# Kernel tuning notes

Measured on AMD Instinct MI355X. Metric: run time of the kernel, lower is better.

Reference implementation:

```python
import jax, jax.numpy as jnp
import numpy as np

N_NODES = 100000
N_EDGES = 1600000
IN_DIM = 128
HEADS = 2
OUT_DIM = 64


def setup_inputs() -> dict:
    key = jax.random.key(0)
    k1, k2, k3, k4, k5 = jax.random.split(key, 5)
    x = jax.random.normal(k1, (N_NODES, IN_DIM), dtype=jnp.float32)
    edge_index = jax.random.randint(k2, (2, N_EDGES), 0, N_NODES, dtype=jnp.int32)
    # xavier-uniform-ish scales
    W = jax.random.uniform(k3, (IN_DIM, HEADS * OUT_DIM), dtype=jnp.float32,
                           minval=-1.0, maxval=1.0) * (6.0 / (IN_DIM + HEADS * OUT_DIM)) ** 0.5
    attn_l = jax.random.uniform(k4, (HEADS, OUT_DIM), dtype=jnp.float32,
                                minval=-1.0, maxval=1.0) * (6.0 / (HEADS + OUT_DIM)) ** 0.5
    attn_r = jax.random.uniform(k5, (HEADS, OUT_DIM), dtype=jnp.float32,
                                minval=-1.0, maxval=1.0) * (6.0 / (HEADS + OUT_DIM)) ** 0.5
    return {"x": x, "edge_index": edge_index, "W": W, "attn_l": attn_l, "attn_r": attn_r}


def reference(x, edge_index, W, attn_l, attn_r):
    N = x.shape[0]
    h = (x @ W).reshape(N, HEADS, OUT_DIM)          # [N,H,D]
    src, dst = edge_index[0], edge_index[1]          # [E]
    h_src = h[src]                                   # [E,H,D] gather
    h_dst = h[dst]                                   # [E,H,D] gather
    # per-edge, per-head attention logits
    alpha = jnp.einsum('ehd,hd->eh', h_src, attn_l) + jnp.einsum('ehd,hd->eh', h_dst, attn_r)
    alpha = jax.nn.leaky_relu(alpha, negative_slope=0.2)
    # NOTE: faithful to original torch code: softmax over dim=0 (ALL edges per head)
    alpha = jax.nn.softmax(alpha, axis=0)            # [E,H]
    msg = h_src * alpha[:, :, None]                  # [E,H,D]
    out = jnp.zeros((N, HEADS, OUT_DIM), dtype=h.dtype).at[dst].add(msg)
    return out.reshape(N, HEADS * OUT_DIM)
```

## Files before the change

### kernel.cpp

```cpp
#include <hip/hip_runtime.h>
#include <hip/hip_fp16.h>
#include <math.h>

#define IN_DIM   128
#define HEADS    2
#define OUT_DIM  64
#define OCOLS    128
#define BSHIFT   7
#define NPB      128
#define MAXB     1024
#define CAPF     2560
#define PARTB    512
#define CHUNK_MAX 3200
#define LOG2E    1.4426950408889634f

typedef __attribute__((ext_vector_type(4))) _Float16 half4v;
typedef __attribute__((ext_vector_type(8))) _Float16 half8v;
typedef __attribute__((ext_vector_type(4))) float    floatx4;

__global__ __launch_bounds__(256) void pack_w_kernel(
    const float* __restrict__ W, half8v* __restrict__ wpack) {
  int t = threadIdx.x;
  for (int s = t; s < 2048; s += 256) {
    int l = s & 63, ct = (s >> 6) & 7, kk = s >> 9;
    int q = l >> 4, n = l & 15;
    int c = ct * 16 + n;
    half8v f;
#pragma unroll
    for (int j = 0; j < 8; j++) {
      f[j] = (_Float16)W[(size_t)(kk * 32 + q * 8 + j) * OCOLS + c];
    }
    wpack[s] = f;
  }
}

__global__ __launch_bounds__(256) void gemm_kernel(
    const float* __restrict__ x, const half8v* __restrict__ wpack,
    const float* __restrict__ attn_l, const float* __restrict__ attn_r,
    _Float16* __restrict__ h16, float* __restrict__ alr, int N) {
  __shared__ half8v Wlds[2048];
  __shared__ __align__(16) _Float16 hstage[64 * OCOLS];
  const int tid = threadIdx.x;
  for (int i = tid; i < 2048; i += 256) Wlds[i] = wpack[i];

  const int wave = tid >> 6, lane = tid & 63;
  const int q = lane >> 4, m = lane & 15;
  const int rbase = blockIdx.x * 64 + wave * 16;
  const int arow = rbase + m;
  const bool rok = arow < N;

  half8v a[4];
#pragma unroll
  for (int kk = 0; kk < 4; kk++) {
    float4 u = rok ? *(const float4*)&x[(size_t)arow * IN_DIM + kk * 32 + q * 8]
                   : make_float4(0.f, 0.f, 0.f, 0.f);
    float4 v = rok ? *(const float4*)&x[(size_t)arow * IN_DIM + kk * 32 + q * 8 + 4]
                   : make_float4(0.f, 0.f, 0.f, 0.f);
    a[kk][0] = (_Float16)u.x; a[kk][1] = (_Float16)u.y;
    a[kk][2] = (_Float16)u.z; a[kk][3] = (_Float16)u.w;
    a[kk][4] = (_Float16)v.x; a[kk][5] = (_Float16)v.y;
    a[kk][6] = (_Float16)v.z; a[kk][7] = (_Float16)v.w;
  }
  __syncthreads();

  floatx4 acc[8];
#pragma unroll
  for (int ct = 0; ct < 8; ct++) {
    floatx4 c = {0.f, 0.f, 0.f, 0.f};
#pragma unroll
    for (int kk = 0; kk < 4; kk++) {
      c = __builtin_amdgcn_mfma_f32_16x16x32_f16(
          a[kk], Wlds[(kk * 8 + ct) * 64 + lane], c, 0, 0, 0);
    }
    acc[ct] = c;
  }

  float Al[8], Ar[8];
#pragma unroll
  for (int ct = 0; ct < 8; ct++) {
    Al[ct] = attn_l[ct * 16 + m];
    Ar[ct] = attn_r[ct * 16 + m];
  }
#pragma unroll
  for (int r = 0; r < 4; r++) {
    float al0 = 0.f, al1 = 0.f, ar0 = 0.f, ar1 = 0.f;
#pragma unroll
    for (int ct = 0; ct < 4; ct++) {
      al0 += acc[ct][r] * Al[ct];
      ar0 += acc[ct][r] * Ar[ct];
      al1 += acc[ct + 4][r] * Al[ct + 4];
      ar1 += acc[ct + 4][r] * Ar[ct + 4];
    }
#pragma unroll
    for (int off = 1; off < 16; off <<= 1) {
      al0 += __shfl_xor(al0, off);
      al1 += __shfl_xor(al1, off);
      ar0 += __shfl_xor(ar0, off);
      ar1 += __shfl_xor(ar1, off);
    }
    int orow = rbase + q * 4 + r;
    if (m == 0 && orow < N) {
      *(float4*)&alr[(size_t)orow * 4] =
          make_float4(al0 * LOG2E, al1 * LOG2E, ar0 * LOG2E, ar1 * LOG2E);
    }
  }

#pragma unroll
  for (int ct = 0; ct < 8; ct++) {
#pragma unroll
    for (int r = 0; r < 4; r++) {
      hstage[(wave * 16 + q * 4 + r) * OCOLS + ct * 16 + m] = (_Float16)acc[ct][r];
    }
  }
  __syncthreads();
  {
    int srow = tid >> 2, seg = tid & 3;
    int grow = blockIdx.x * 64 + srow;
    if (grow < N) {
      const int4* s = (const int4*)&hstage[srow * OCOLS + seg * 32];
      int4* d = (int4*)&h16[(size_t)grow * OCOLS + seg * 32];
      int4 v0 = s[0], v1 = s[1], v2 = s[2], v3 = s[3];
      d[0] = v0; d[1] = v1; d[2] = v2; d[3] = v3;
    }
  }
}

__device__ inline void softmax_comb(float& m, float& s, float m2, float s2) {
  float M = fmaxf(m, m2);
  s = s * __builtin_amdgcn_exp2f(m - M) + s2 * __builtin_amdgcn_exp2f(m2 - M);
  m = M;
}

__global__ __launch_bounds__(512) void alpha_part_kernel(
    const int* __restrict__ src, const int* __restrict__ dst,
    const float* __restrict__ alr, float* __restrict__ partials,
    int* __restrict__ gcur, unsigned int* __restrict__ pairs,
    int E, int nb1, int chunk) {
  __shared__ unsigned int pv[CHUNK_MAX];
  __shared__ unsigned short bk[CHUNK_MAX];
  __shared__ int hist[MAXB];
  __shared__ int cur[MAXB];
  const int t = threadIdx.x;
  const int base = blockIdx.x * chunk;
  const int lim = min(base + chunk, E);
  const int cntLoc = lim - base;

  for (int i = t; i < nb1; i += 512) hist[i] = 0;
  __syncthreads();

  const char* ab = (const char*)alr;
  float m0 = -1e30f, s0 = 0.f, m1 = -1e30f, s1 = 0.f;
  for (int e = base + t; e < lim; e += 512) {
    int sn = src[e], dn = dst[e];
    int li = e - base;
    pv[li] = (unsigned int)sn | ((unsigned int)(dn & (NPB - 1)) << 17);
    bk[li] = (unsigned short)(dn >> BSHIFT);
    atomicAdd(&hist[dn >> BSHIFT], 1);
    float4 as = *(const float4*)(ab + ((unsigned)sn << 4));
    float4 ad = *(const float4*)(ab + ((unsigned)dn << 4));
    float a0 = as.x + ad.z;
    float a1 = as.y + ad.w;
    a0 = (a0 > 0.f) ? a0 : 0.2f * a0;
    a1 = (a1 > 0.f) ? a1 : 0.2f * a1;
    {
      float M = fmaxf(m0, a0);
      s0 = s0 * __builtin_amdgcn_exp2f(m0 - M) + __builtin_amdgcn_exp2f(a0 - M);
      m0 = M;
    }
    {
      float M = fmaxf(m1, a1);
      s1 = s1 * __builtin_amdgcn_exp2f(m1 - M) + __builtin_amdgcn_exp2f(a1 - M);
      m1 = M;
    }
  }
  __syncthreads();
  for (int b = t; b < nb1; b += 512) {
    int h = hist[b];
    if (h) cur[b] = b * CAPF + atomicAdd(&gcur[b], h);
  }
  __syncthreads();
  for (int li = t; li < cntLoc; li += 512) {
    unsigned int p = pv[li];
    int bb = bk[li];
    int slot = atomicAdd(&cur[bb], 1);
    int cap = (bb + 1) * CAPF - 1;
    if (slot > cap) slot = cap;
    pairs[slot] = p;
  }
#pragma unroll
  for (int off = 1; off < 64; off <<= 1) {
    float m0o = __shfl_xor(m0, off), s0o = __shfl_xor(s0, off);
    float m1o = __shfl_xor(m1, off), s1o = __shfl_xor(s1, off);
    softmax_comb(m0, s0, m0o, s0o);
    softmax_comb(m1, s1, m1o, s1o);
  }
  __shared__ float red[8][4];
  int wave = t >> 6, lane = t & 63;
  if (lane == 0) {
    red[wave][0] = m0; red[wave][1] = s0; red[wave][2] = m1; red[wave][3] = s1;
  }
  __syncthreads();
  if (t == 0) {
    float M0 = red[0][0], S0 = red[0][1], M1 = red[0][2], S1 = red[0][3];
    for (int w = 1; w < 8; w++) {
      softmax_comb(M0, S0, red[w][0], red[w][1]);
      softmax_comb(M1, S1, red[w][2], red[w][3]);
    }
    float* p = &partials[(size_t)blockIdx.x * 4];
    p[0] = M0; p[1] = S0; p[2] = M1; p[3] = S1;
  }
}

__global__ __launch_bounds__(512) void stats_kernel(
    const float* __restrict__ partials, float* __restrict__ stats) {
  __shared__ float red[8][4];
  int t = threadIdx.x;
  float m0 = -1e30f, s0 = 0.f, m1 = -1e30f, s1 = 0.f;
  for (int i = t; i < PARTB; i += 512) {
    const float* p = &partials[(size_t)i * 4];
    softmax_comb(m0, s0, p[0], p[1]);
    softmax_comb(m1, s1, p[2], p[3]);
  }
#pragma unroll
  for (int off = 1; off < 64; off <<= 1) {
    float m0o = __shfl_xor(m0, off), s0o = __shfl_xor(s0, off);
    float m1o = __shfl_xor(m1, off), s1o = __shfl_xor(s1, off);
    softmax_comb(m0, s0, m0o, s0o);
    softmax_comb(m1, s1, m1o, s1o);
  }
  int wave = t >> 6, lane = t & 63;
  if (lane == 0) {
    red[wave][0] = m0; red[wave][1] = s0; red[wave][2] = m1; red[wave][3] = s1;
  }
  __syncthreads();
  if (t == 0) {
    float M0 = red[0][0], S0 = red[0][1], M1 = red[0][2], S1 = red[0][3];
    for (int w = 1; w < 8; w++) {
      softmax_comb(M0, S0, red[w][0], red[w][1]);
      softmax_comb(M1, S1, red[w][2], red[w][3]);
    }
    stats[0] = M0; stats[1] = 1.f / S0;
    stats[2] = M1; stats[3] = 1.f / S1;
  }
}

__global__ __launch_bounds__(512) void csr_gather_kernel(
    const unsigned int* __restrict__ pairs, const int* __restrict__ gcur,
    const float* __restrict__ alr, const float* __restrict__ stats,
    const _Float16* __restrict__ h16, float* __restrict__ out, int N) {
  __shared__ int buf[CAPF];
  __shared__ int cnt[NPB], excl[NPB], cur[NPB];
  const int b = blockIdx.x, t = threadIdx.x;
  const int base_node = b << BSHIFT;
  const int rb = b * CAPF;
  int cntE = gcur[b];
  if (cntE > CAPF) cntE = CAPF;

  if (t < NPB) cnt[t] = 0;
  __syncthreads();
  for (int i = t; i < cntE; i += 512) {
    atomicAdd(&cnt[pairs[rb + i] >> 17], 1);
  }
  __syncthreads();
  if (t < NPB) excl[t] = cnt[t];
  __syncthreads();
  for (int d = 1; d < NPB; d <<= 1) {
    int x = 0;
    if (t < NPB && t >= d) x = excl[t - d];
    __syncthreads();
    if (t < NPB) excl[t] += x;
    __syncthreads();
  }
  if (t < NPB) {
    int e = excl[t] - cnt[t];
    excl[t] = e;
    cur[t] = e;
  }
  __syncthreads();
  for (int i = t; i < cntE; i += 512) {
    unsigned int p = pairs[rb + i];
    int slot = atomicAdd(&cur[p >> 17], 1);
    buf[slot] = (int)(p & 0x1FFFFu);
  }
  __syncthreads();

  const int wave = t >> 6, lane = t & 63;
  const int sub = lane >> 4;
  const int l = lane & 15;
  const int head = l >> 3;
  const char* ab = (const char*)alr;
  const char* hb = (const char*)h16;
  const float M = stats[head * 2];
  const float invS = stats[head * 2 + 1];
  const unsigned loff = (unsigned)l * 16u;

  for (int k = 0; k < NPB / 8; k++) {
    int nl = wave + 8 * k;
    int n = base_node + nl;
    if (n >= N) break;
    float4 ad = *(const float4*)(ab + ((unsigned)n << 4));
    float adv = head ? ad.w : ad.z;
    int beg = excl[nl], end = beg + cnt[nl];
    float acc[8] = {0.f, 0.f, 0.f, 0.f, 0.f, 0.f, 0.f, 0.f};
    for (int ib = beg + sub; ib < end; ib += 16) {
      bool k1 = ib + 4 < end, k2 = ib + 8 < end, k3 = ib + 12 < end;
      int sn0 = buf[ib];
      int sn1 = buf[k1 ? ib + 4 : ib];
      int sn2 = buf[k2 ? ib + 8 : ib];
      int sn3 = buf[k3 ? ib + 12 : ib];
      float4 as0 = *(const float4*)(ab + ((unsigned)sn0 << 4));
      float4 as1 = *(const float4*)(ab + ((unsigned)sn1 << 4));
      float4 as2 = *(const float4*)(ab + ((unsigned)sn2 << 4));
      float4 as3 = *(const float4*)(ab + ((unsigned)sn3 << 4));
      half8v hv0 = *(const half8v*)(hb + (((unsigned)sn0 << 8) + loff));
      half8v hv1 = *(const half8v*)(hb + (((unsigned)sn1 << 8) + loff));
      half8v hv2 = *(const half8v*)(hb + (((unsigned)sn2 << 8) + loff));
      half8v hv3 = *(const half8v*)(hb + (((unsigned)sn3 << 8) + loff));
      float a0 = (head ? as0.y : as0.x) + adv;
      float a1 = (head ? as1.y : as1.x) + adv;
      float a2 = (head ? as2.y : as2.x) + adv;
      float a3 = (head ? as3.y : as3.x) + adv;
      a0 = (a0 > 0.f) ? a0 : 0.2f * a0;
      a1 = (a1 > 0.f) ? a1 : 0.2f * a1;
      a2 = (a2 > 0.f) ? a2 : 0.2f * a2;
      a3 = (a3 > 0.f) ? a3 : 0.2f * a3;
      float w0 = __builtin_amdgcn_exp2f(a0 - M) * invS;
      float w1 = k1 ? __builtin_amdgcn_exp2f(a1 - M) * invS : 0.f;
      float w2 = k2 ? __builtin_amdgcn_exp2f(a2 - M) * invS : 0.f;
      float w3 = k3 ? __builtin_amdgcn_exp2f(a3 - M) * invS : 0.f;
#pragma unroll
      for (int j = 0; j < 8; j++) acc[j] += w0 * (float)hv0[j];
#pragma unroll
      for (int j = 0; j < 8; j++) acc[j] += w1 * (float)hv1[j];
#pragma unroll
      for (int j = 0; j < 8; j++) acc[j] += w2 * (float)hv2[j];
#pragma unroll
      for (int j = 0; j < 8; j++) acc[j] += w3 * (float)hv3[j];
    }
#pragma unroll
    for (int j = 0; j < 8; j++) {
      acc[j] += __shfl_xor(acc[j], 16);
      acc[j] += __shfl_xor(acc[j], 32);
    }
    if (sub == 0) {
      char* ob = (char*)out;
      unsigned obase = ((unsigned)n << 9) + (unsigned)l * 32u;
      floatx4 o0 = {acc[0], acc[1], acc[2], acc[3]};
      floatx4 o1 = {acc[4], acc[5], acc[6], acc[7]};
      __builtin_nontemporal_store(o0, (floatx4*)(ob + obase));
      __builtin_nontemporal_store(o1, (floatx4*)(ob + obase + 16));
    }
  }
}

extern "C" void kernel_launch(void* const* d_in, const int* in_sizes, int n_in,
                              void* d_out, int out_size, void* d_ws, size_t ws_size,
                              hipStream_t stream) {
  const float* x      = (const float*)d_in[0];
  const int*   edge   = (const int*)d_in[1];
  const float* W      = (const float*)d_in[2];
  const float* attn_l = (const float*)d_in[3];
  const float* attn_r = (const float*)d_in[4];

  const int N = in_sizes[0] / IN_DIM;
  const int E = in_sizes[1] / 2;
  const int* src = edge;
  const int* dst = edge + E;
  float* out = (float*)d_out;

  const int nb1 = (N + NPB - 1) >> BSHIFT;

  _Float16*     h16      = (_Float16*)d_ws;
  float*        alr      = (float*)(h16 + (size_t)N * OCOLS);
  float*        partials = alr + (size_t)N * 4;
  float*        stats    = partials + (size_t)PARTB * 4;
  int*          gcur     = (int*)(stats + 4);
  unsigned int* pairs    = (unsigned int*)(gcur + MAXB);
  half8v*       wpack    = (half8v*)(pairs + (size_t)nb1 * CAPF);

  int chunk = (E + PARTB - 1) / PARTB;
  if (chunk > CHUNK_MAX) chunk = CHUNK_MAX;

  hipMemsetAsync(gcur, 0, MAXB * sizeof(int), stream);

  pack_w_kernel<<<1, 256, 0, stream>>>(W, wpack);
  gemm_kernel<<<(N + 63) / 64, 256, 0, stream>>>(x, wpack, attn_l, attn_r, h16, alr, N);
  alpha_part_kernel<<<PARTB, 512, 0, stream>>>(src, dst, alr, partials, gcur,
                                               pairs, E, nb1, chunk);
  stats_kernel<<<1, 512, 0, stream>>>(partials, stats);
  csr_gather_kernel<<<nb1, 512, 0, stream>>>(pairs, gcur, alr, stats, h16, out, N);
}
```

Measured before the change: 257.7 us.

## Fuse W packing, gcur reset and softmax stats into neighbouring kernels

Removes the pack_w kernel, the memset and the stats kernel, cutting the launch count from five to three. Each GEMM block now converts W to fp16 into LDS itself, and block 0 clears gcur. Every gather block recomputes the global softmax stats from the partials and caches its edge pairs in LDS so the second scan reads LDS instead of global memory. In exchange, W conversion and the stats reduction are repeated in every block, and LDS use in the gather kernel grows, which may lower occupancy.

```diff
diff --git a/kernel.cpp b/kernel.cpp
--- a/kernel.cpp
+++ b/kernel.cpp
@@ -18,10 +18,18 @@
 typedef __attribute__((ext_vector_type(8))) _Float16 half8v;
 typedef __attribute__((ext_vector_type(4))) float    floatx4;
 
-__global__ __launch_bounds__(256) void pack_w_kernel(
-    const float* __restrict__ W, half8v* __restrict__ wpack) {
-  int t = threadIdx.x;
-  for (int s = t; s < 2048; s += 256) {
+__global__ __launch_bounds__(256) void gemm_kernel(
+    const float* __restrict__ x, const float* __restrict__ W,
+    const float* __restrict__ attn_l, const float* __restrict__ attn_r,
+    _Float16* __restrict__ h16, float* __restrict__ alr,
+    int* __restrict__ gcur, int N) {
+  __shared__ half8v Wlds[2048];
+  __shared__ __align__(16) _Float16 hstage[64 * OCOLS];
+  const int tid = threadIdx.x;
+  if (blockIdx.x == 0) {
+    for (int i = tid; i < MAXB; i += 256) gcur[i] = 0;
+  }
+  for (int s = tid; s < 2048; s += 256) {
     int l = s & 63, ct = (s >> 6) & 7, kk = s >> 9;
     int q = l >> 4, n = l & 15;
     int c = ct * 16 + n;
@@ -30,18 +38,8 @@
     for (int j = 0; j < 8; j++) {
       f[j] = (_Float16)W[(size_t)(kk * 32 + q * 8 + j) * OCOLS + c];
     }
-    wpack[s] = f;
-  }
-}
-
-__global__ __launch_bounds__(256) void gemm_kernel(
-    const float* __restrict__ x, const half8v* __restrict__ wpack,
-    const float* __restrict__ attn_l, const float* __restrict__ attn_r,
-    _Float16* __restrict__ h16, float* __restrict__ alr, int N) {
-  __shared__ half8v Wlds[2048];
-  __shared__ __align__(16) _Float16 hstage[64 * OCOLS];
-  const int tid = threadIdx.x;
-  for (int i = tid; i < 2048; i += 256) Wlds[i] = wpack[i];
+    Wlds[s] = f;
+  }
 
   const int wave = tid >> 6, lane = tid & 63;
   const int q = lane >> 4, m = lane & 15;
@@ -211,45 +209,14 @@
   }
 }
 
-__global__ __launch_bounds__(512) void stats_kernel(
-    const float* __restrict__ partials, float* __restrict__ stats) {
-  __shared__ float red[8][4];
-  int t = threadIdx.x;
-  float m0 = -1e30f, s0 = 0.f, m1 = -1e30f, s1 = 0.f;
-  for (int i = t; i < PARTB; i += 512) {
-    const float* p = &partials[(size_t)i * 4];
-    softmax_comb(m0, s0, p[0], p[1]);
-    softmax_comb(m1, s1, p[2], p[3]);
-  }
-#pragma unroll
-  for (int off = 1; off < 64; off <<= 1) {
-    float m0o = __shfl_xor(m0, off), s0o = __shfl_xor(s0, off);
-    float m1o = __shfl_xor(m1, off), s1o = __shfl_xor(s1, off);
-    softmax_comb(m0, s0, m0o, s0o);
-    softmax_comb(m1, s1, m1o, s1o);
-  }
-  int wave = t >> 6, lane = t & 63;
-  if (lane == 0) {
-    red[wave][0] = m0; red[wave][1] = s0; red[wave][2] = m1; red[wave][3] = s1;
-  }
-  __syncthreads();
-  if (t == 0) {
-    float M0 = red[0][0], S0 = red[0][1], M1 = red[0][2], S1 = red[0][3];
-    for (int w = 1; w < 8; w++) {
-      softmax_comb(M0, S0, red[w][0], red[w][1]);
-      softmax_comb(M1, S1, red[w][2], red[w][3]);
-    }
-    stats[0] = M0; stats[1] = 1.f / S0;
-    stats[2] = M1; stats[3] = 1.f / S1;
-  }
-}
-
 __global__ __launch_bounds__(512) void csr_gather_kernel(
     const unsigned int* __restrict__ pairs, const int* __restrict__ gcur,
-    const float* __restrict__ alr, const float* __restrict__ stats,
+    const float* __restrict__ alr, const float* __restrict__ partials,
     const _Float16* __restrict__ h16, float* __restrict__ out, int N) {
+  __shared__ int praw[CAPF];
   __shared__ int buf[CAPF];
   __shared__ int cnt[NPB], excl[NPB], cur[NPB];
+  __shared__ float sstat[4];
   const int b = blockIdx.x, t = threadIdx.x;
   const int base_node = b << BSHIFT;
   const int rb = b * CAPF;
@@ -257,9 +224,30 @@
   if (cntE > CAPF) cntE = CAPF;
 
   if (t < NPB) cnt[t] = 0;
+  if (t < 64) {
+    float m0 = -1e30f, s0 = 0.f, m1 = -1e30f, s1 = 0.f;
+    for (int i = t; i < PARTB; i += 64) {
+      const float* p = &partials[(size_t)i * 4];
+      softmax_comb(m0, s0, p[0], p[1]);
+      softmax_comb(m1, s1, p[2], p[3]);
+    }
+#pragma unroll
+    for (int off = 1; off < 64; off <<= 1) {
+      float m0o = __shfl_xor(m0, off), s0o = __shfl_xor(s0, off);
+      float m1o = __shfl_xor(m1, off), s1o = __shfl_xor(s1, off);
+      softmax_comb(m0, s0, m0o, s0o);
+      softmax_comb(m1, s1, m1o, s1o);
+    }
+    if (t == 0) {
+      sstat[0] = m0; sstat[1] = 1.f / s0;
+      sstat[2] = m1; sstat[3] = 1.f / s1;
+    }
+  }
   __syncthreads();
   for (int i = t; i < cntE; i += 512) {
-    atomicAdd(&cnt[pairs[rb + i] >> 17], 1);
+    unsigned int p = pairs[rb + i];
+    praw[i] = (int)p;
+    atomicAdd(&cnt[p >> 17], 1);
   }
   __syncthreads();
   if (t < NPB) excl[t] = cnt[t];
@@ -278,7 +266,7 @@
   }
   __syncthreads();
   for (int i = t; i < cntE; i += 512) {
-    unsigned int p = pairs[rb + i];
+    unsigned int p = (unsigned int)praw[i];
     int slot = atomicAdd(&cur[p >> 17], 1);
     buf[slot] = (int)(p & 0x1FFFFu);
   }
@@ -290,8 +278,8 @@
   const int head = l >> 3;
   const char* ab = (const char*)alr;
   const char* hb = (const char*)h16;
-  const float M = stats[head * 2];
-  const float invS = stats[head * 2 + 1];
+  const float M = sstat[head * 2];
+  const float invS = sstat[head * 2 + 1];
   const unsigned loff = (unsigned)l * 16u;
 
   for (int k = 0; k < NPB / 8; k++) {
@@ -373,20 +361,15 @@
   _Float16*     h16      = (_Float16*)d_ws;
   float*        alr      = (float*)(h16 + (size_t)N * OCOLS);
   float*        partials = alr + (size_t)N * 4;
-  float*        stats    = partials + (size_t)PARTB * 4;
-  int*          gcur     = (int*)(stats + 4);
+  int*          gcur     = (int*)(partials + (size_t)PARTB * 4);
   unsigned int* pairs    = (unsigned int*)(gcur + MAXB);
-  half8v*       wpack    = (half8v*)(pairs + (size_t)nb1 * CAPF);
 
   int chunk = (E + PARTB - 1) / PARTB;
   if (chunk > CHUNK_MAX) chunk = CHUNK_MAX;
 
-  hipMemsetAsync(gcur, 0, MAXB * sizeof(int), stream);
-
-  pack_w_kernel<<<1, 256, 0, stream>>>(W, wpack);
-  gemm_kernel<<<(N + 63) / 64, 256, 0, stream>>>(x, wpack, attn_l, attn_r, h16, alr, N);
+  gemm_kernel<<<(N + 63) / 64, 256, 0, stream>>>(x, W, attn_l, attn_r, h16, alr,
+                                                 gcur, N);
   alpha_part_kernel<<<PARTB, 512, 0, stream>>>(src, dst, alr, partials, gcur,
                                                pairs, E, nb1, chunk);
-  stats_kernel<<<1, 512, 0, stream>>>(partials, stats);
-  csr_gather_kernel<<<nb1, 512, 0, stream>>>(pairs, gcur, alr, stats, h16, out, N);
-}
+  csr_gather_kernel<<<nb1, 512, 0, stream>>>(pairs, gcur, alr, partials, h16, out, N);
+}
```

Measured after the change: 252.8 us. No clear change (-1.9%).
